# Kernel tuning notes

Measured on AMD Instinct MI355X. Metric: run time of the kernel, lower is better.

Reference implementation:

```python
import jax, jax.numpy as jnp
import numpy as np

LOSS_IDX = jnp.array([0, 1])    # loss_indices from __init__
BASIS_IDX = jnp.array([0, 1])   # dtw_mapping_basis (x, y)


def _dtw_path(cost):
    """Classic DTW DP + backtrack on cost [N, M].
    Returns padded alignment path (a, b) of length N+M-1 with validity mask.
    DP is run as an anti-diagonal wavefront scan (L = N+M-1 steps)."""
    N, M = cost.shape
    L = N + M - 1
    inf = jnp.float32(jnp.inf)
    i_idx = jnp.arange(N)

    def diag_step(carry, k):
        prev1, prev2 = carry  # diagonals k-1 and k-2, indexed by row i
        j = k - i_idx
        valid = (j >= 0) & (j < M)
        c = cost[i_idx, jnp.clip(j, 0, M - 1)]
        up = jnp.concatenate([jnp.full((1,), inf), prev1[:-1]])  # D[i-1, j]
        dg = jnp.concatenate([jnp.full((1,), inf), prev2[:-1]])  # D[i-1, j-1]
        lf = prev1                                               # D[i, j-1]
        best = jnp.minimum(jnp.minimum(up, dg), lf)
        best = jnp.where(jnp.isinf(best), jnp.float32(0.0), best)  # (0,0) seed
        cur = jnp.where(valid, c + best, inf)
        return (cur, prev1), cur

    init = (jnp.full((N,), inf), jnp.full((N,), inf))
    _, diags = jax.lax.scan(diag_step, init, jnp.arange(L))  # [L, N]: D[i,j] = diags[i+j, i]

    def getD(i, j):
        ok = (i >= 0) & (j >= 0)
        return jnp.where(ok, diags[jnp.clip(i + j, 0, L - 1), jnp.clip(i, 0, N - 1)], inf)

    def bt_step(carry, _):
        i, j, done = carry
        emit_valid = jnp.logical_not(done)
        cand = jnp.stack([getD(i - 1, j - 1), getD(i - 1, j), getD(i, j - 1)])
        m = jnp.argmin(cand)  # 0: diag, 1: up, 2: left
        ni = jnp.where(m == 2, i, i - 1)
        nj = jnp.where(m == 1, j, j - 1)
        done2 = done | ((i == 0) & (j == 0))
        ni = jnp.where(done2, 0, ni)
        nj = jnp.where(done2, 0, nj)
        return (ni, nj, done2), (i, j, emit_valid)

    init_bt = (jnp.int32(N - 1), jnp.int32(M - 1), jnp.bool_(False))
    _, (a, b, valid) = jax.lax.scan(bt_step, init_bt, None, length=L)
    return a, b, valid


def _dtw_loss_single(pred, targ, subcoef):
    # DTW alignment is computed on detached (numpy in torch) basis coords.
    p = jax.lax.stop_gradient(pred)[:, BASIS_IDX]
    t = jax.lax.stop_gradient(targ)[:, BASIS_IDX]
    # euclidean pairwise distance cost [N, M]
    cost = jnp.sqrt(jnp.sum((p[:, None, :] - t[None, :, :]) ** 2, axis=-1))
    a, b, valid = _dtw_path(cost)
    d = jnp.abs(pred[a][:, LOSS_IDX] - targ[b][:, LOSS_IDX]) * subcoef  # [L, 2]
    return jnp.sum(d * valid[:, None].astype(d.dtype))


def setup_inputs() -> dict:
    key = jax.random.key(0)
    k1, k2 = jax.random.split(key)
    B, N, M, F = 32, 1024, 1024, 4
    preds = jax.random.normal(k1, (B, N, F), dtype=jnp.float32)
    targs = jax.random.normal(k2, (B, M, F), dtype=jnp.float32)
    subcoef = jnp.ones((2,), dtype=jnp.float32)
    return {"preds": preds, "targs": targs, "subcoef": subcoef}


def reference(preds, targs, subcoef):
    per_sample = jax.vmap(_dtw_loss_single, in_axes=(0, 0, None))(preds, targs, subcoef)
    return jnp.sum(per_sample)
```

## Files before the change

kernel.cpp:

```cpp
#include <hip/hip_runtime.h>
#include <math.h>

#define BATCH 32
#define NN 1024
#define MM 1024
#define LPATH (NN + MM - 1)

#define PB 128
#define PQ 128
#define GB 8
#define GH 8
#define PAN_WORDS 1536
#define BAT_WORDS (GB * GH * PAN_WORDS)
#define RCPL (9 * 1024)
#define RC_OFFW ((size_t)BATCH * BAT_WORDS)
#define BR_OFFW (RC_OFFW + (size_t)BATCH * RCPL)
#define WS_WORDS (BR_OFFW + (size_t)BATCH * RCPL)
#define REQ_WS_NEW (WS_WORDS * 4)

#define DEC_WORDS_PER_BATCH ((NN / 4) * (MM / 4))
#define REQ_WS ((size_t)BATCH * DEC_WORDS_PER_BATCH * 4)

__global__ void init_kernel(float* out) { out[0] = 0.0f; }

__global__ void init2(float* __restrict__ ws, float* __restrict__ out)
{
    const int b = blockIdx.x, t = threadIdx.x;
    const float INF = __builtin_inff();
    if (b == 0 && t == 0) out[0] = 0.0f;
    float* rc0 = ws + RC_OFFW + (size_t)b * RCPL;
    float* br0 = ws + BR_OFFW + (size_t)b * RCPL;
    for (int i = t; i < 1024; i += 256) { rc0[i] = INF; br0[i] = INF; }
}

__global__ __launch_bounds__(64, 1) void dtw_panel(
    const float* __restrict__ preds, const float* __restrict__ targs,
    float* __restrict__ ws, const int diag)
{
    const int b = blockIdx.y;
    const int r0 = (diag > GH - 1) ? diag - (GH - 1) : 0;
    const int r = r0 + blockIdx.x;
    const int c = diag - r;
    const int l = threadIdx.x;
    const float INF = __builtin_inff();

    __shared__ __align__(16) float txP[260], tyP[260];
    __shared__ __align__(16) float TL[200];
    __shared__ __align__(16) float botL[128];

    if (l < 63) { txP[l] = 0.f; tyP[l] = 0.f; }
    txP[191 + l] = 0.f; tyP[191 + l] = 0.f;
    if (l < 6) { txP[255 + l] = 0.f; tyP[255 + l] = 0.f; }
    TL[128 + l] = INF; if (l < 8) TL[192 + l] = INF;

    const float4* tg4 = (const float4*)targs + (size_t)b * MM + c * PQ;
    {
        const float4 a = tg4[l], e = tg4[64 + l];
        txP[63 + l] = a.x;      tyP[63 + l] = a.y;
        txP[63 + 64 + l] = e.x; tyP[63 + 64 + l] = e.y;
    }
    const float* browR = ws + BR_OFFW + ((size_t)b * 9 + r) * 1024 + c * PQ;
    TL[l] = browR[l]; TL[64 + l] = browR[64 + l];

    const float4* pp4 = (const float4*)preds + (size_t)b * NN + r * PB;
    const float4 p0 = pp4[2 * l], p1 = pp4[2 * l + 1];
    const float px0 = p0.x, py0 = p0.y, px1 = p1.x, py1 = p1.y;

    const float* rc = ws + RC_OFFW + ((size_t)b * 9 + c) * 1024 + r * PB;
    float D0 = rc[2 * l], D1 = rc[2 * l + 1];
    const float corner = (c == 0) ? ((r == 0) ? 0.0f : INF) : browR[-1];
    const float dg0init = (l == 0) ? corner : rc[2 * l - 1];

    unsigned* __restrict__ decP = (unsigned*)ws + (size_t)b * BAT_WORDS
                                + (size_t)(r * GH + c) * PAN_WORDS + l;
    __syncthreads();

    float txb[8], tyb[8];
    #pragma unroll
    for (int k = 0; k < 4; ++k) { txb[k] = txP[63 + k - l]; tyb[k] = tyP[63 + k - l]; }
    float up0prev = INF;

    for (int it = 0; it < 24; ++it) {
        const int s0 = it * 8;
        const float4 T4a = *(const float4*)&TL[s0];
        const float4 T4b = *(const float4*)&TL[s0 + 4];
        const float Tv[8] = {T4a.x, T4a.y, T4a.z, T4a.w,
                             T4b.x, T4b.y, T4b.z, T4b.w};
        unsigned word = 0;
        #pragma unroll
        for (int k = 0; k < 8; ++k) {
            const int s = s0 + k;
            const int jq = s - l;
            txb[(k + 4) & 7] = txP[63 + jq + 4];
            tyb[(k + 4) & 7] = tyP[63 + jq + 4];
            const float sh = __shfl_up(D1, 1);
            const float up0 = (l == 0) ? Tv[k] : sh;
            const float dg0 = (jq == 0) ? dg0init : up0prev;
            const float tx = txb[k], ty = tyb[k];
            const float dx0 = px0 - tx, dy0 = py0 - ty;
            const float c0 = __builtin_amdgcn_sqrtf(dx0 * dx0 + dy0 * dy0);
            const float mn0 = fminf(dg0, fminf(up0, D0));
            const float D0n = c0 + mn0;
            const unsigned m0 = (mn0 == dg0) ? 0u : ((mn0 == up0) ? 1u : 2u);
            const float dg1 = D0;
            const float dx1 = px1 - tx, dy1 = py1 - ty;
            const float c1 = __builtin_amdgcn_sqrtf(dx1 * dx1 + dy1 * dy1);
            const float mn1 = fminf(dg1, fminf(D0n, D1));
            const float D1n = c1 + mn1;
            const unsigned m1 = (mn1 == dg1) ? 0u : ((mn1 == D0n) ? 1u : 2u);
            word |= (m0 | (m1 << 2)) << (4 * k);
            const bool act = (jq >= 0) && (jq < PQ);
            if (act) { D0 = D0n; D1 = D1n; }
            up0prev = up0;
            if (l == 63 && act) botL[jq] = D1n;
        }
        decP[it * 64] = word;
    }

    float* rcw = ws + RC_OFFW + ((size_t)b * 9 + (c + 1)) * 1024 + r * PB;
    rcw[2 * l] = D0; rcw[2 * l + 1] = D1;
    __syncthreads();
    float* brw = ws + BR_OFFW + ((size_t)b * 9 + (r + 1)) * 1024 + c * PQ;
    brw[l] = botL[l]; brw[64 + l] = botL[64 + l];
}

__global__ __launch_bounds__(256, 1) void dtw_bt(
    const float* __restrict__ preds, const float* __restrict__ targs,
    const float* __restrict__ subcoef, const float* __restrict__ ws,
    float* __restrict__ out)
{
    const int b = blockIdx.x, t = threadIdx.x;
    __shared__ float pxA[NN], pyA[NN], txA[MM], tyA[MM];
    __shared__ __align__(16) unsigned sdec[24576];
    __shared__ unsigned path[2048];
    __shared__ int sI, sJ, sN;
    __shared__ float wsum[4];

    for (int it = 0; it < 4; ++it) {
        const int idx = it * 256 + t;
        const float4 p4 = ((const float4*)preds)[(size_t)b * NN + idx];
        pxA[idx] = p4.x; pyA[idx] = p4.y;
        const float4 t4 = ((const float4*)targs)[(size_t)b * MM + idx];
        txA[idx] = t4.x; tyA[idx] = t4.y;
    }
    if (t == 0) { sI = NN - 1; sJ = MM - 1; sN = 0; }

    const unsigned* decB = (const unsigned*)ws + (size_t)b * BAT_WORDS;
    for (int pair = 3; pair >= 0; --pair) {
        __syncthreads();
        const uint4* g4 = (const uint4*)(decB + (size_t)pair * 24576);
        uint4* s4 = (uint4*)sdec;
        for (int k = t; k < 6144; k += 256) s4[k] = g4[k];
        __syncthreads();
        if (t == 0) {
            int i = sI, j = sJ, n = sN;
            const int iLow = pair * 256;
            if (i >= iLow) {
                int cwidx = -1; unsigned cw = 0;
                while (true) {
                    path[n++] = ((unsigned)i << 16) | (unsigned)j;
                    if ((i | j) == 0) { i = -1; break; }
                    const int rr = i >> 7, cc = j >> 7;
                    const int ll = (i & 127) >> 1;
                    const int ss = ll + (j & 127);
                    const int widx = ((rr - 2 * pair) * GH + cc) * PAN_WORDS
                                   + (ss >> 3) * 64 + ll;
                    if (widx != cwidx) { cw = sdec[widx]; cwidx = widx; }
                    const unsigned m = (cw >> ((ss & 7) * 4 + (i & 1) * 2)) & 3u;
                    i -= (m != 2u); j -= (m != 1u);
                    if (i < iLow) break;
                }
            }
            sI = i; sJ = j; sN = n;
        }
    }
    __syncthreads();

    const float sc0 = subcoef[0], sc1 = subcoef[1];
    const int n = sN;
    float acc = 0.0f;
    for (int p = t; p < n; p += 256) {
        const unsigned e = path[p];
        const int i = (int)(e >> 16), j = (int)(e & 0xffffu);
        acc += fabsf(pxA[i] - txA[j]) * sc0 + fabsf(pyA[i] - tyA[j]) * sc1;
    }
    #pragma unroll
    for (int o = 32; o > 0; o >>= 1) acc += __shfl_down(acc, o);
    if ((t & 63) == 0) wsum[t >> 6] = acc;
    __syncthreads();
    if (t == 0) atomicAdd(out, (wsum[0] + wsum[1]) + (wsum[2] + wsum[3]));
}

__device__ inline void bt_walk4(const unsigned* __restrict__ sdec, int roff,
                                int iLow, int& i, int& j, int& n,
                                unsigned* __restrict__ path)
{
    int ri = i >> 2, jc = j >> 2;
    unsigned w = sdec[(ri - roff) * 256 + jc];
    while (true) {
        const int base = (ri - roff) * 256 + jc;
        const unsigned wl = sdec[(jc > 0)    ? base - 1   : base];
        const unsigned wu = sdec[(ri > roff) ? base - 256 : base];
        const unsigned wd = sdec[(ri > roff && jc > 0) ? base - 257 : base];
        bool done = false, susp = false;
        while (true) {
            path[n++] = ((unsigned)i << 16) | (unsigned)j;
            if ((i | j) == 0) { done = true; break; }
            const unsigned m = (w >> (((i & 3) * 4 + (j & 3)) * 2)) & 3u;
            i -= (m != 2u); j -= (m != 1u);
            if (i < iLow) { susp = true; break; }
            if ((i >> 2) != ri || (j >> 2) != jc) break;
        }
        if (done || susp) break;
        const int nri = i >> 2, njc = j >> 2;
        w = (nri == ri) ? wl : ((njc == jc) ? wu : wd);
        ri = nri; jc = njc;
    }
}

#define RRL 4
#define CCL 4
#define LANES 64
#define NWAVE 4
#define TPBL (MM / 4)
#define NSUP (TPBL + LANES - 1)
#define LAG 72
#define TOTL (NSUP + (NWAVE - 1) * LAG)
#define DEPTH 32

__global__ __launch_bounds__(256, 1) void dtw_fused_legacy(
    const float* __restrict__ preds, const float* __restrict__ targs,
    const float* __restrict__ subcoef, unsigned* __restrict__ dec,
    float* __restrict__ out)
{
    const int b = blockIdx.x, t = threadIdx.x;
    const int l = t & 63, w = t >> 6;
    const float INF = __builtin_inff();

    __shared__ float pxA[NN], pyA[NN], txA[MM], tyA[MM];
    __shared__ float4 ring[NWAVE - 1][DEPTH];
    __shared__ unsigned sdec[128 * 256];
    __shared__ unsigned path[LPATH + 1];
    __shared__ int sI, sJ, sN;
    __shared__ float wsum[NWAVE];

    for (int it = 0; it < NN / 256; ++it) {
        const int idx = it * 256 + t;
        const float4 p4 = ((const float4*)preds)[(size_t)b * NN + idx];
        pxA[idx] = p4.x; pyA[idx] = p4.y;
        const float4 t4 = ((const float4*)targs)[(size_t)b * MM + idx];
        txA[idx] = t4.x; tyA[idx] = t4.y;
    }
    __syncthreads();

    const int i0 = (w << 8) + (l << 2);
    const float4 px4 = ((const float4*)pxA)[i0 >> 2];
    const float4 py4 = ((const float4*)pyA)[i0 >> 2];
    const float px[RRL] = {px4.x, px4.y, px4.z, px4.w};
    const float py[RRL] = {py4.x, py4.y, py4.z, py4.w};
    unsigned* __restrict__ decW =
        dec + (size_t)b * DEC_WORDS_PER_BATCH + ((size_t)w << 14) + (size_t)l;

    float Dp[RRL], Dbot[CCL], bv[CCL];
    #pragma unroll
    for (int r = 0; r < RRL; ++r) Dp[r] = INF;
    #pragma unroll
    for (int c = 0; c < CCL; ++c) { Dbot[c] = INF; bv[c] = INF; }
    float bndRet = (w == 0 && l == 0) ? 0.0f : INF;
    float4 gcur = make_float4(INF, INF, INF, INF);
    float4 tx4 = ((const float4*)txA)[0], ty4 = ((const float4*)tyA)[0];
    const float4* __restrict__ ringR = ring[(w > 0) ? (w - 1) : 0];

    for (int u = 0; u < TOTL; ++u) {
        const int ul = u - LAG * w;
        if (l == 0) {
            const bool gb = (w > 0) && (ul >= 0) && (ul < TPBL);
            bv[0] = gb ? gcur.x : INF; bv[1] = gb ? gcur.y : INF;
            bv[2] = gb ? gcur.z : INF; bv[3] = gb ? gcur.w : INF;
        }
        const bool act = (ul >= l) && (ul < l + TPBL);
        if (act) {
            const float cx[CCL] = {tx4.x, tx4.y, tx4.z, tx4.w};
            const float cy[CCL] = {ty4.x, ty4.y, ty4.z, ty4.w};
            float cost[RRL][CCL];
            #pragma unroll
            for (int c = 0; c < CCL; ++c)
                #pragma unroll
                for (int r = 0; r < RRL; ++r) {
                    const float dx = px[r] - cx[c], dy = py[r] - cy[c];
                    cost[r][c] = __builtin_amdgcn_sqrtf(dx * dx + dy * dy);
                }
            unsigned word = 0;
            #pragma unroll
            for (int c = 0; c < CCL; ++c) {
                float up = bv[c];
                float dg = (c == 0) ? bndRet : bv[c - 1];
                #pragma unroll
                for (int r = 0; r < RRL; ++r) {
                    const float lf = Dp[r];
                    const unsigned m = (dg <= up && dg <= lf) ? 0u
                                     : ((up <= lf) ? 1u : 2u);
                    const float D = cost[r][c] + fminf(dg, fminf(up, lf));
                    word |= m << ((r * 4 + c) * 2);
                    dg = lf; up = D; Dp[r] = D;
                }
                Dbot[c] = up;
            }
            decW[(ul & 255) << 6] = word;
            if (l == LANES - 1 && w < NWAVE - 1)
                ring[w][ul & (DEPTH - 1)] =
                    make_float4(Dbot[0], Dbot[1], Dbot[2], Dbot[3]);
        }
        bndRet = bv[CCL - 1];
        #pragma unroll
        for (int c = 0; c < CCL; ++c) bv[c] = __shfl_up(Dbot[c], 1);
        const int un = ul + 1;
        if (un >= l && un < l + TPBL) {
            const int jn = CCL * (un - l);
            tx4 = ((const float4*)txA)[jn >> 2];
            ty4 = ((const float4*)tyA)[jn >> 2];
        }
        if (w > 0 && un >= 0 && un < TPBL)
            gcur = ringR[(un + 63) & (DEPTH - 1)];
        if ((u & 7) == 7) __syncthreads();
    }

    __threadfence_block();
    __syncthreads();

    const unsigned* __restrict__ decB = dec + (size_t)b * DEC_WORDS_PER_BATCH;
    {
        const uint4* g4 = (const uint4*)(decB + 32768);
        for (int k = t; k < 8192; k += 256) {
            const uint4 v = g4[k];
            const int kb = k << 2;
            const int wv = kb >> 14;
            const int rem = kb & 16383;
            const int q = rem >> 6;
            const int lb = rem & 63;
            const unsigned wd[4] = {v.x, v.y, v.z, v.w};
            #pragma unroll
            for (int e = 0; e < 4; ++e) {
                const int ll = lb + e;
                const int row = (wv << 6) + ll;
                const int jc = (q - ll) & 255;
                sdec[(row << 8) + jc] = wd[e];
            }
        }
    }
    __syncthreads();
    if (t == 0) {
        int i = NN - 1, j = MM - 1, n = 0;
        bt_walk4(sdec, 128, 512, i, j, n, path);
        sI = i; sJ = j; sN = n;
    }
    __syncthreads();
    {
        const uint4* g4 = (const uint4*)decB;
        for (int k = t; k < 8192; k += 256) {
            const uint4 v = g4[k];
            const int kb = k << 2;
            const int wv = kb >> 14;
            const int rem = kb & 16383;
            const int q = rem >> 6;
            const int lb = rem & 63;
            const unsigned wd[4] = {v.x, v.y, v.z, v.w};
            #pragma unroll
            for (int e = 0; e < 4; ++e) {
                const int ll = lb + e;
                const int row = (wv << 6) + ll;
                const int jc = (q - ll) & 255;
                sdec[(row << 8) + jc] = wd[e];
            }
        }
    }
    __syncthreads();
    if (t == 0) {
        int i = sI, j = sJ, n = sN;
        bt_walk4(sdec, 0, 0, i, j, n, path);
        sN = n;
    }
    __syncthreads();

    const float sc0 = subcoef[0], sc1 = subcoef[1];
    const int n = sN;
    float acc = 0.0f;
    for (int p = t; p < n; p += 256) {
        const unsigned e = path[p];
        const int i = (int)(e >> 16), j = (int)(e & 0xffffu);
        acc += fabsf(pxA[i] - txA[j]) * sc0 + fabsf(pyA[i] - tyA[j]) * sc1;
    }
    #pragma unroll
    for (int o = 32; o > 0; o >>= 1) acc += __shfl_down(acc, o);
    if ((t & 63) == 0) wsum[t >> 6] = acc;
    __syncthreads();
    if (t == 0) atomicAdd(out, (wsum[0] + wsum[1]) + (wsum[2] + wsum[3]));
}

__global__ __launch_bounds__(256) void dtw_fallback(
    const float* __restrict__ preds, const float* __restrict__ targs,
    const float* __restrict__ subcoef, unsigned* __restrict__ dec,
    float* __restrict__ out)
{
    const int b = blockIdx.x;
    const int t = threadIdx.x;
    const float INF = __builtin_inff();
    __shared__ float px[NN], py[NN];
    __shared__ float txy[2 * MM];
    __shared__ float bbuf[2][256];

    for (int it = 0; it < NN / 256; ++it) {
        const int idx = it * 256 + t;
        const float4 p4 = ((const float4*)preds)[(size_t)b * NN + idx];
        px[idx] = p4.x; py[idx] = p4.y;
        const float4 t4 = ((const float4*)targs)[(size_t)b * MM + idx];
        txy[2 * idx] = t4.x; txy[2 * idx + 1] = t4.y;
    }
    bbuf[0][t] = INF; bbuf[1][t] = INF;
    __syncthreads();

    float pxr[4], pyr[4], Dp[4];
    #pragma unroll
    for (int r = 0; r < 4; ++r) {
        pxr[r] = px[4 * t + r]; pyr[r] = py[4 * t + r]; Dp[r] = INF;
    }
    float dgB = (t == 0) ? 0.0f : INF;
    unsigned packed = 0;
    unsigned* decB = dec + (size_t)b * 65536;
    for (int s = 0; s < MM + 255; ++s) {
        const int j = s - t;
        const float upB = (t == 0) ? INF : bbuf[(s + 1) & 1][t - 1];
        if (j >= 0 && j < MM) {
            const float txj = txy[2 * j], tyj = txy[2 * j + 1];
            float up = upB, dg = dgB;
            unsigned mbits = 0;
            #pragma unroll
            for (int r = 0; r < 4; ++r) {
                const float dx = pxr[r] - txj, dy = pyr[r] - tyj;
                const float c = sqrtf(dx * dx + dy * dy);
                const float lf = Dp[r];
                const unsigned m = (dg <= up && dg <= lf) ? 0u
                                 : ((up <= lf) ? 1u : 2u);
                mbits |= m << (r * 8 + (j & 3) * 2);
                const float Dc = c + fminf(up, fminf(dg, lf));
                dg = lf; up = Dc; Dp[r] = Dc;
            }
            packed |= mbits;
            if ((j & 3) == 3) { decB[(unsigned)t * 256 + (j >> 2)] = packed; packed = 0; }
            bbuf[s & 1][t] = Dp[3];
        }
        dgB = upB;
        __syncthreads();
    }
    __threadfence_block();
    __syncthreads();
    if (t == 0) {
        const float sc0 = subcoef[0], sc1 = subcoef[1];
        int i = NN - 1, jj = MM - 1;
        float loss = 0.0f;
        int ti = i >> 2, tj = jj >> 2;
        unsigned wv = decB[ti * 256 + tj];
        while (true) {
            const int tjl = (tj > 0) ? tj - 1 : 0;
            const int til = (ti > 0) ? ti - 1 : 0;
            const unsigned wl = decB[ti * 256 + tjl];
            const unsigned wu = decB[til * 256 + tj];
            const unsigned wd = decB[til * 256 + tjl];
            bool done = false;
            while (true) {
                loss += fabsf(px[i] - txy[2 * jj]) * sc0
                      + fabsf(py[i] - txy[2 * jj + 1]) * sc1;
                if ((i | jj) == 0) { done = true; break; }
                const unsigned m = (wv >> (((i & 3) * 4 + (jj & 3)) * 2)) & 3u;
                i -= (m != 2u); jj -= (m != 1u);
                if ((i >> 2) != ti || (jj >> 2) != tj) break;
            }
            if (done) break;
            const int nti = i >> 2, ntj = jj >> 2;
            wv = (nti == ti) ? wl : ((ntj == tj) ? wu : wd);
            ti = nti; tj = ntj;
        }
        atomicAdd(out, loss);
    }
}

extern "C" void kernel_launch(void* const* d_in, const int* in_sizes, int n_in,
                              void* d_out, int out_size, void* d_ws, size_t ws_size,
                              hipStream_t stream) {
    const float* preds   = (const float*)d_in[0];
    const float* targs   = (const float*)d_in[1];
    const float* subcoef = (const float*)d_in[2];
    float* out = (float*)d_out;

    if (ws_size >= REQ_WS_NEW) {
        float* wsf = (float*)d_ws;
        init2<<<BATCH, 256, 0, stream>>>(wsf, out);
        for (int d = 0; d < GB + GH - 1; ++d) {
            const int r0 = (d > GH - 1) ? d - (GH - 1) : 0;
            const int r1 = (d < GB - 1) ? d : GB - 1;
            dim3 grid(r1 - r0 + 1, BATCH);
            dtw_panel<<<grid, 64, 0, stream>>>(preds, targs, wsf, d);
        }
        dtw_bt<<<BATCH, 256, 0, stream>>>(preds, targs, subcoef, wsf, out);
    } else if (ws_size >= REQ_WS) {
        unsigned* dec = (unsigned*)d_ws;
        init_kernel<<<1, 1, 0, stream>>>(out);
        dtw_fused_legacy<<<BATCH, 256, 0, stream>>>(preds, targs, subcoef, dec, out);
    } else {
        unsigned* dec = (unsigned*)d_ws;
        init_kernel<<<1, 1, 0, stream>>>(out);
        dtw_fallback<<<BATCH, 256, 0, stream>>>(preds, targs, subcoef, dec, out);
    }
}
```

Measured before the change: 578.5 us.

## Backtrack directly from global decision words and use DPP lane shift in panel

The backtrack kernel no longer stages 96KB chunks of decision words into shared memory with block-wide copies and syncs. A single thread now walks the path reading decision words straight from global memory, relying on the cache and on reusing the same word across steps. In the DP panel, __shfl_up is replaced with a DPP wave_shr1 row shift. The direct reads put global latency on the serial backtrack walk, and the DPP control 0x138 has to behave as a full-wave shift right by one, or lane 0 of each row gets the wrong value.

```diff
diff --git a/kernel.cpp b/kernel.cpp
--- a/kernel.cpp
+++ b/kernel.cpp
@@ -31,6 +31,12 @@
     float* rc0 = ws + RC_OFFW + (size_t)b * RCPL;
     float* br0 = ws + BR_OFFW + (size_t)b * RCPL;
     for (int i = t; i < 1024; i += 256) { rc0[i] = INF; br0[i] = INF; }
+}
+
+__device__ __forceinline__ float wave_shr1(float v)
+{
+    return __int_as_float(__builtin_amdgcn_update_dpp(
+        __float_as_int(v), __float_as_int(v), 0x138, 0xF, 0xF, false));
 }
 
 __global__ __launch_bounds__(64, 1) void dtw_panel(
@@ -93,7 +99,7 @@
             const int jq = s - l;
             txb[(k + 4) & 7] = txP[63 + jq + 4];
             tyb[(k + 4) & 7] = tyP[63 + jq + 4];
-            const float sh = __shfl_up(D1, 1);
+            const float sh = wave_shr1(D1);
             const float up0 = (l == 0) ? Tv[k] : sh;
             const float dg0 = (jq == 0) ? dg0init : up0prev;
             const float tx = txb[k], ty = tyb[k];
@@ -131,9 +137,8 @@
 {
     const int b = blockIdx.x, t = threadIdx.x;
     __shared__ float pxA[NN], pyA[NN], txA[MM], tyA[MM];
-    __shared__ __align__(16) unsigned sdec[24576];
     __shared__ unsigned path[2048];
-    __shared__ int sI, sJ, sN;
+    __shared__ int sN;
     __shared__ float wsum[4];
 
     for (int it = 0; it < 4; ++it) {
@@ -143,36 +148,25 @@
         const float4 t4 = ((const float4*)targs)[(size_t)b * MM + idx];
         txA[idx] = t4.x; tyA[idx] = t4.y;
     }
-    if (t == 0) { sI = NN - 1; sJ = MM - 1; sN = 0; }
-
-    const unsigned* decB = (const unsigned*)ws + (size_t)b * BAT_WORDS;
-    for (int pair = 3; pair >= 0; --pair) {
-        __syncthreads();
-        const uint4* g4 = (const uint4*)(decB + (size_t)pair * 24576);
-        uint4* s4 = (uint4*)sdec;
-        for (int k = t; k < 6144; k += 256) s4[k] = g4[k];
-        __syncthreads();
-        if (t == 0) {
-            int i = sI, j = sJ, n = sN;
-            const int iLow = pair * 256;
-            if (i >= iLow) {
-                int cwidx = -1; unsigned cw = 0;
-                while (true) {
-                    path[n++] = ((unsigned)i << 16) | (unsigned)j;
-                    if ((i | j) == 0) { i = -1; break; }
-                    const int rr = i >> 7, cc = j >> 7;
-                    const int ll = (i & 127) >> 1;
-                    const int ss = ll + (j & 127);
-                    const int widx = ((rr - 2 * pair) * GH + cc) * PAN_WORDS
-                                   + (ss >> 3) * 64 + ll;
-                    if (widx != cwidx) { cw = sdec[widx]; cwidx = widx; }
-                    const unsigned m = (cw >> ((ss & 7) * 4 + (i & 1) * 2)) & 3u;
-                    i -= (m != 2u); j -= (m != 1u);
-                    if (i < iLow) break;
-                }
-            }
-            sI = i; sJ = j; sN = n;
-        }
+    __syncthreads();
+
+    if (t == 0) {
+        const unsigned* __restrict__ decB =
+            (const unsigned*)ws + (size_t)b * BAT_WORDS;
+        int i = NN - 1, j = MM - 1, n = 0;
+        int cwidx = -1; unsigned cw = 0;
+        while (true) {
+            path[n++] = ((unsigned)i << 16) | (unsigned)j;
+            if ((i | j) == 0) break;
+            const int ll = (i & 127) >> 1;
+            const int ss = ll + (j & 127);
+            const int widx = (((i >> 7) << 3) + (j >> 7)) * PAN_WORDS
+                           + (ss >> 3) * 64 + ll;
+            if (widx != cwidx) { cw = decB[widx]; cwidx = widx; }
+            const unsigned m = (cw >> ((ss & 7) * 4 + (i & 1) * 2)) & 3u;
+            i -= (m != 2u); j -= (m != 1u);
+        }
+        sN = n;
     }
     __syncthreads();
 
```

After: 540.3 us. -6.6%, faster.
